# Performance work log

Measured on AMD Instinct MI355X. Metric: run time of the kernel, lower is better.

Reference implementation:

```python
import jax, jax.numpy as jnp
import numpy as np
from jax import lax

NUM_HEADS = 8
NUM_SELECTS = 10
CLIP = 10.0  # tanh logit clipping in pointer-style SingleHeadAttention
NEG = -1e9   # finite -inf substitute (safe under autodiff)


def setup_inputs() -> dict:
    key = jax.random.key(0)
    ks = jax.random.split(key, 8)
    B, N, D = 64, 2048, 256
    s = 1.0 / np.sqrt(D)
    return {
        "encoder_output": jax.random.normal(ks[0], (B, N, D), jnp.float32),
        "in_proj_w": jax.random.uniform(ks[1], (3 * D, D), jnp.float32, -s, s),
        "in_proj_b": jnp.zeros((3 * D,), jnp.float32),
        "out_w": jax.random.uniform(ks[2], (D, D), jnp.float32, -s, s),
        "out_b": jnp.zeros((D,), jnp.float32),
        "sha_wq": jax.random.uniform(ks[3], (D, D), jnp.float32, -s, s),
        "sha_wk": jax.random.uniform(ks[4], (D, D), jnp.float32, -s, s),
        "is_training": False,
    }


def reference(encoder_output, in_proj_w, in_proj_b, out_w, out_b, sha_wq, sha_wk, is_training):
    B, N, D = encoder_output.shape
    H, dh, S = NUM_HEADS, D // NUM_HEADS, NUM_SELECTS
    Wq, Wk, Wv = in_proj_w[:D], in_proj_w[D:2 * D], in_proj_w[2 * D:]
    bq, bk, bv = in_proj_b[:D], in_proj_b[D:2 * D], in_proj_b[2 * D:]

    h_mean = jnp.mean(encoder_output, axis=1)                         # [B,D]
    # MHA query is constant across steps; K/V projections of the encoder too.
    q = (h_mean @ Wq.T + bq).reshape(B, H, dh)                        # [B,H,dh]
    k = (encoder_output @ Wk.T + bk).reshape(B, N, H, dh)             # [B,N,H,dh]
    v = (encoder_output @ Wv.T + bv).reshape(B, N, H, dh)             # [B,N,H,dh]
    ksingle = encoder_output @ sha_wk.T                               # [B,N,D]
    scale = 1.0 / np.sqrt(dh)
    scale2 = 1.0 / np.sqrt(D)
    bidx = jnp.arange(B)

    def step(mask, _):
        # multi-head cross attention, key_padding_mask = mask
        s_mha = jnp.einsum('bhd,bnhd->bhn', q, k) * scale             # [B,H,N]
        s_mha = jnp.where(mask[:, None, :], NEG, s_mha)
        a = jax.nn.softmax(s_mha, axis=-1)
        ctx = jnp.einsum('bhn,bnhd->bhd', a, v).reshape(B, D)
        attn_out = ctx @ out_w.T + out_b                              # [B,D]
        # single-head pointer attention with tanh clipping
        qs = attn_out @ sha_wq.T                                      # [B,D]
        u = CLIP * jnp.tanh(jnp.einsum('bd,bnd->bn', qs, ksingle) * scale2)
        u = jnp.where(mask, NEG, u)                                   # [B,N]
        logp = jax.nn.log_softmax(u, axis=-1)
        p = jnp.exp(logp)
        ent = -jnp.sum(jnp.where(p > 0, p * logp, 0.0), axis=-1)
        # is_training=False path: greedy argmax (deterministic reference)
        idx = jnp.argmax(p, axis=-1)                                  # [B]
        pi_s = p[bidx, idx]
        new_mask = mask.at[bidx, idx].set(True)
        return new_mask, (idx, pi_s, ent)

    mask0 = jnp.zeros((B, N), dtype=bool)
    _, (idxs, pis, ents) = lax.scan(step, mask0, None, length=S)
    selected_clients = idxs.T.astype(jnp.int64 if jax.config.jax_enable_x64 else jnp.int32)  # [B,S]
    pi = pis.T                                                        # [B,S]
    entropy = jnp.sum(ents, axis=0)                                   # [B]
    return selected_clients, pi, entropy
```

## Files before the change

kernel.cpp:

```cpp
#include <hip/hip_runtime.h>
#include <hip/hip_bf16.h>
#include <math.h>

namespace {
constexpr int Bc = 64, Nc = 2048, Dc = 256, Hc = 8, DHc = 32, Sc = 10;
constexpr float kNeg = -1000000000.0f;
constexpr float kClip = 10.0f;
constexpr float kScale = 0.17677669529663687f;
constexpr float kScale2 = 0.0625f;
}

__global__ __launch_bounds__(256) void k_hmean_part(const float* __restrict__ enc,
                                                    float* __restrict__ hpart) {
  int b = blockIdx.x >> 3, c = blockIdx.x & 7, t = threadIdx.x;
  int lane = t & 63, wv = t >> 6;
  __shared__ __align__(16) float part[4][Dc];
  const float4* p = reinterpret_cast<const float4*>(
      enc + ((size_t)b * Nc + c * 256 + wv * 64) * Dc) + lane;
  float4 s; s.x = 0.f; s.y = 0.f; s.z = 0.f; s.w = 0.f;
  #pragma unroll 8
  for (int i = 0; i < 64; ++i) {
    const float4 e = p[(size_t)i * 64];
    s.x += e.x; s.y += e.y; s.z += e.z; s.w += e.w;
  }
  *reinterpret_cast<float4*>(&part[wv][lane * 4]) = s;
  __syncthreads();
  hpart[(size_t)blockIdx.x * Dc + t] =
      part[0][t] + part[1][t] + part[2][t] + part[3][t];
}

__global__ __launch_bounds__(256) void k_qgc(const float* __restrict__ hpart,
                                             const float* __restrict__ w_in,
                                             const float* __restrict__ b_in,
                                             float* __restrict__ g, float* __restrict__ c) {
  int b = blockIdx.x, t = threadIdx.x;
  __shared__ float hm[Dc];
  __shared__ float qsh[Dc];
  {
    float s = 0.f;
    for (int cc = 0; cc < 8; ++cc) s += hpart[(size_t)(b * 8 + cc) * Dc + t];
    hm[t] = s * (1.0f / Nc);
  }
  __syncthreads();
  {
    const float* row = w_in + (size_t)t * Dc;
    float acc = b_in[t];
    for (int d = 0; d < Dc; ++d) acc += row[d] * hm[d];
    qsh[t] = acc;
  }
  __syncthreads();
  for (int h = 0; h < Hc; ++h) {
    float acc = 0.f;
    const float* wk = w_in + (size_t)(Dc + h * DHc) * Dc + t;
    const float* qh = qsh + h * DHc;
    #pragma unroll 8
    for (int i = 0; i < DHc; ++i) acc += qh[i] * wk[(size_t)i * Dc];
    g[((size_t)b * Hc + h) * Dc + t] = acc;
  }
  if (t < Hc) {
    float acc = 0.f;
    for (int i = 0; i < DHc; ++i) acc += qsh[t * DHc + i] * b_in[Dc + t * DHc + i];
    c[b * Hc + t] = acc;
  }
}

__global__ __launch_bounds__(256) void k_A1(const float* __restrict__ swq,
                                            const float* __restrict__ ow,
                                            const float* __restrict__ ob,
                                            float* __restrict__ M1, float* __restrict__ m1b) {
  int i = blockIdx.x, e = threadIdx.x;
  __shared__ float row[Dc];
  __shared__ float red[256];
  row[e] = swq[(size_t)i * Dc + e];
  __syncthreads();
  float acc = 0.f;
  #pragma unroll 4
  for (int k = 0; k < Dc; ++k) acc += row[k] * ow[(size_t)k * Dc + e];
  M1[(size_t)i * Dc + e] = acc;
  red[e] = row[e] * ob[e];
  __syncthreads();
  for (int off = 128; off >= 1; off >>= 1) {
    if (e < off) red[e] += red[e + off];
    __syncthreads();
  }
  if (e == 0) m1b[i] = red[0];
}

__global__ __launch_bounds__(256) void k_A2(const float* __restrict__ swk,
                                            const float* __restrict__ M1,
                                            const float* __restrict__ m1b,
                                            const float* __restrict__ b_in,
                                            float* __restrict__ Aout, float* __restrict__ cvec) {
  int d = blockIdx.x, e = threadIdx.x;
  __shared__ float col[Dc];
  __shared__ float red[256];
  col[e] = swk[(size_t)e * Dc + d];
  __syncthreads();
  float acc = 0.f;
  #pragma unroll 4
  for (int k = 0; k < Dc; ++k) acc += col[k] * M1[(size_t)k * Dc + e];
  Aout[(size_t)d * Dc + e] = acc;
  red[e] = acc * b_in[2 * Dc + e] + col[e] * m1b[e];
  __syncthreads();
  for (int off = 128; off >= 1; off >>= 1) {
    if (e < off) red[e] += red[e + off];
    __syncthreads();
  }
  if (e == 0) cvec[d] = red[0];
}

__global__ __launch_bounds__(256) void k_A3(const float* __restrict__ Aout,
                                            const float* __restrict__ w_in,
                                            float* __restrict__ BT) {
  int h = blockIdx.x >> 3, et = blockIdx.x & 7, d = threadIdx.x;
  float arow[DHc];
  #pragma unroll
  for (int i = 0; i < DHc; ++i) arow[i] = Aout[(size_t)d * Dc + h * DHc + i];
  __shared__ float wv[DHc][DHc];
  for (int k = threadIdx.x; k < DHc * DHc; k += 256) {
    int i = k >> 5, j = k & 31;
    wv[i][j] = w_in[(size_t)(2 * Dc + h * DHc + i) * Dc + et * DHc + j];
  }
  __syncthreads();
  for (int j = 0; j < DHc; ++j) {
    float acc = 0.f;
    #pragma unroll
    for (int i = 0; i < DHc; ++i) acc += arow[i] * wv[i][j];
    BT[((size_t)h * Dc + et * DHc + j) * Dc + d] = acc;
  }
}

__global__ __launch_bounds__(256) void k_scores(const float* __restrict__ enc,
                                                const float* __restrict__ g,
                                                const float* __restrict__ c,
                                                float* __restrict__ s) {
  int b = blockIdx.x >> 4, nt = blockIdx.x & 15, t = threadIdx.x;
  __shared__ __align__(16) float gsm[Hc * Dc];
  __shared__ float csm[Hc];
  for (int k = t; k < Hc * Dc; k += 256) gsm[k] = g[(size_t)b * Hc * Dc + k];
  if (t < Hc) csm[t] = c[b * Hc + t];
  __syncthreads();
  int row = t >> 1, half = t & 1;
  int n = nt * 128 + row;
  const float4* rowp = reinterpret_cast<const float4*>(enc + ((size_t)b * Nc + n) * Dc);
  float acc[Hc] = {};
  #pragma unroll 8
  for (int i = 0; i < 32; ++i) {
    int d4 = i * 2 + half;
    const float4 e = rowp[d4];
    #pragma unroll
    for (int h = 0; h < Hc; ++h) {
      const float4 g4 = *reinterpret_cast<const float4*>(gsm + h * Dc + d4 * 4);
      acc[h] += e.x * g4.x + e.y * g4.y + e.z * g4.z + e.w * g4.w;
    }
  }
  #pragma unroll
  for (int h = 0; h < Hc; ++h) acc[h] += __shfl_xor(acc[h], 1);
  if (half == 0) {
    #pragma unroll
    for (int h = 0; h < Hc; ++h)
      s[((size_t)b * Hc + h) * Nc + n] = kScale * (acc[h] + csm[h]);
  }
}

__global__ __launch_bounds__(256) void k_rowmax(const float* __restrict__ s,
                                                float* __restrict__ mrow) {
  int bh = blockIdx.x, t = threadIdx.x;
  __shared__ float red[256];
  float m = -3.0e38f;
  #pragma unroll
  for (int q = 0; q < 8; ++q) m = fmaxf(m, s[(size_t)bh * Nc + q * 256 + t]);
  red[t] = m;
  __syncthreads();
  for (int off = 128; off >= 1; off >>= 1) {
    if (t < off) red[t] = fmaxf(red[t], red[t + off]);
    __syncthreads();
  }
  if (t == 0) mrow[bh] = red[0];
}

__global__ __launch_bounds__(256) void k_S0part(const float* __restrict__ enc,
                                                const float* __restrict__ s,
                                                const float* __restrict__ mrow,
                                                float* __restrict__ w,
                                                float* __restrict__ Spart) {
  int b = blockIdx.x >> 3, cid = blockIdx.x & 7, t = threadIdx.x;
  __shared__ __align__(16) float wsmT[256 * 8];
  __shared__ __align__(16) float part[4][Hc][Dc];
  {
    float eh[8];
    #pragma unroll
    for (int h = 0; h < Hc; ++h) {
      float m = mrow[b * Hc + h];
      float e = expf(s[((size_t)b * Hc + h) * Nc + cid * 256 + t] - m);
      eh[h] = e;
      w[((size_t)b * Hc + h) * Nc + cid * 256 + t] = e;
    }
    float4 v0; v0.x = eh[0]; v0.y = eh[1]; v0.z = eh[2]; v0.w = eh[3];
    float4 v1; v1.x = eh[4]; v1.y = eh[5]; v1.z = eh[6]; v1.w = eh[7];
    *reinterpret_cast<float4*>(&wsmT[t * 8]) = v0;
    *reinterpret_cast<float4*>(&wsmT[t * 8 + 4]) = v1;
  }
  __syncthreads();
  int lane = t & 63, wv = t >> 6;
  float4 acc[Hc];
  #pragma unroll
  for (int h = 0; h < Hc; ++h) { acc[h].x = 0.f; acc[h].y = 0.f; acc[h].z = 0.f; acc[h].w = 0.f; }
  const float4* ep = reinterpret_cast<const float4*>(
      enc + ((size_t)b * Nc + cid * 256 + wv * 64) * Dc) + lane;
  for (int i = 0; i < 64; ++i) {
    const float4 e4 = ep[(size_t)i * 64];
    int row = wv * 64 + i;
    const float4 w0 = *reinterpret_cast<const float4*>(&wsmT[row * 8]);
    const float4 w1 = *reinterpret_cast<const float4*>(&wsmT[row * 8 + 4]);
    const float wh[8] = {w0.x, w0.y, w0.z, w0.w, w1.x, w1.y, w1.z, w1.w};
    #pragma unroll
    for (int h = 0; h < Hc; ++h) {
      acc[h].x += wh[h] * e4.x; acc[h].y += wh[h] * e4.y;
      acc[h].z += wh[h] * e4.z; acc[h].w += wh[h] * e4.w;
    }
  }
  #pragma unroll
  for (int h = 0; h < Hc; ++h)
    *reinterpret_cast<float4*>(&part[wv][h][lane * 4]) = acc[h];
  __syncthreads();
  #pragma unroll
  for (int h = 0; h < Hc; ++h)
    Spart[(((size_t)b * 8 + cid) * Hc + h) * Dc + t] =
        part[0][h][t] + part[1][h][t] + part[2][h][t] + part[3][h][t];
}

__global__ __launch_bounds__(256) void k_S0red(const float* __restrict__ Spart,
                                               const float* __restrict__ w,
                                               float* __restrict__ Sacc,
                                               float* __restrict__ W0) {
  int b = blockIdx.x >> 3, h = blockIdx.x & 7, t = threadIdx.x;
  __shared__ float red[256];
  float acc = 0.f;
  for (int cid = 0; cid < 8; ++cid)
    acc += Spart[(((size_t)b * 8 + cid) * Hc + h) * Dc + t];
  Sacc[((size_t)b * Hc + h) * Dc + t] = acc;
  float ws = 0.f;
  #pragma unroll
  for (int q = 0; q < 8; ++q) ws += w[((size_t)b * Hc + h) * Nc + q * 256 + t];
  red[t] = ws;
  __syncthreads();
  for (int off = 128; off >= 1; off >>= 1) {
    if (t < off) red[t] += red[t + off];
    __syncthreads();
  }
  if (t == 0) W0[b * Hc + h] = red[0];
}

__device__ __forceinline__ void select_core(const float* __restrict__ ub,
                                            const int* histsh, int nhist, int t,
                                            float* red, int* redi,
                                            int& gidx_out, float& lse_out, float& ent_out) {
  float uval[8];
  float lmax = -3.0e38f;
  int lidx = 0;
  #pragma unroll
  for (int q = 0; q < 8; ++q) {
    int n = t + q * 256;
    float v = ub[n];
    for (int tt = 0; tt < nhist; ++tt)
      if (n == histsh[tt]) v = kNeg;
    uval[q] = v;
    if (v > lmax) { lmax = v; lidx = n; }
  }
  red[t] = lmax; redi[t] = lidx;
  __syncthreads();
  for (int off = 128; off >= 1; off >>= 1) {
    if (t < off) {
      float o = red[t + off]; int oi = redi[t + off];
      if (o > red[t] || (o == red[t] && oi < redi[t])) { red[t] = o; redi[t] = oi; }
    }
    __syncthreads();
  }
  float mu = red[0];
  int gidx = redi[0];
  __syncthreads();
  float ssum = 0.f;
  #pragma unroll
  for (int q = 0; q < 8; ++q) ssum += expf(uval[q] - mu);
  red[t] = ssum;
  __syncthreads();
  for (int off = 128; off >= 1; off >>= 1) {
    if (t < off) red[t] += red[t + off];
    __syncthreads();
  }
  float Z = red[0];
  float lse = mu + logf(Z);
  __syncthreads();
  float ent = 0.f;
  #pragma unroll
  for (int q = 0; q < 8; ++q) {
    float logp = uval[q] - lse;
    float p = expf(logp);
    if (p > 0.f) ent -= p * logp;
  }
  red[t] = ent;
  __syncthreads();
  for (int off = 128; off >= 1; off >>= 1) {
    if (t < off) red[t] += red[t + off];
    __syncthreads();
  }
  ent_out = red[0];
  gidx_out = gidx;
  lse_out = lse;
  __syncthreads();
}

__global__ __launch_bounds__(256) void k_selchain(const float* __restrict__ u,
                                                  int* __restrict__ hist,
                                                  float* __restrict__ out,
                                                  const float* __restrict__ Sacc,
                                                  const float* __restrict__ W0,
                                                  const float* __restrict__ w,
                                                  const float* __restrict__ enc,
                                                  const float* __restrict__ BT,
                                                  float* __restrict__ rpart, int tstep) {
  int b = blockIdx.x >> 3, h = blockIdx.x & 7, t = threadIdx.x;
  __shared__ float red[256];
  __shared__ int redi[256];
  __shared__ int histsh[16];
  __shared__ float sh[Dc];
  if (t < 16) histsh[t] = (t < tstep - 1) ? hist[b * 16 + t] : -1;
  __syncthreads();

  if (tstep > 0) {
    int sel_t = tstep - 1;
    int gidx; float lse, ent;
    select_core(u + (size_t)b * Nc, histsh, sel_t, t, red, redi, gidx, lse, ent);
    if (h == 0 && t == 0) {
      float pi = expf(u[(size_t)b * Nc + gidx] - lse);
      out[b * Sc + sel_t] = (float)gidx;
      out[Bc * Sc + b * Sc + sel_t] = pi;
      if (sel_t == 0) out[2 * Bc * Sc + b] = ent;
      else out[2 * Bc * Sc + b] += ent;
      hist[b * 16 + sel_t] = gidx;
    }
    if (t == 0) histsh[sel_t] = gidx;
    __syncthreads();
  }

  float se = Sacc[((size_t)b * Hc + h) * Dc + t];
  float Wh = W0[b * Hc + h];
  for (int tt = 0; tt < tstep; ++tt) {
    int j = histsh[tt];
    float wv = w[((size_t)b * Hc + h) * Nc + j];
    se -= wv * enc[((size_t)b * Nc + j) * Dc + t];
    Wh -= wv;
  }
  sh[t] = se / Wh;
  __syncthreads();
  const float* bt = BT + (size_t)h * Dc * Dc + t;
  float a0 = 0.f, a1 = 0.f, a2 = 0.f, a3 = 0.f;
  #pragma unroll 4
  for (int e = 0; e < Dc; e += 4) {
    a0 += bt[(size_t)e * Dc] * sh[e];
    a1 += bt[(size_t)(e + 1) * Dc] * sh[e + 1];
    a2 += bt[(size_t)(e + 2) * Dc] * sh[e + 2];
    a3 += bt[(size_t)(e + 3) * Dc] * sh[e + 3];
  }
  rpart[((size_t)b * Hc + h) * Dc + t] = (a0 + a1) + (a2 + a3);
}

__global__ __launch_bounds__(256) void k_uscore(const float* __restrict__ enc,
                                                const float* __restrict__ rpart,
                                                const float* __restrict__ cvec,
                                                float* __restrict__ u) {
  int b = blockIdx.x >> 5, ng = blockIdx.x & 31, t = threadIdx.x;
  __shared__ __align__(16) float rsm[Dc];
  {
    float vsum = cvec[t];
    #pragma unroll
    for (int h = 0; h < Hc; ++h) vsum += rpart[((size_t)b * Hc + h) * Dc + t];
    rsm[t] = vsum;
  }
  __syncthreads();
  int row = t >> 2, q = t & 3;
  int n = ng * 64 + row;
  const float4* rowp = reinterpret_cast<const float4*>(enc + ((size_t)b * Nc + n) * Dc);
  const float4* r4 = reinterpret_cast<const float4*>(rsm);
  float acc = 0.f;
  #pragma unroll
  for (int i = 0; i < 16; ++i) {
    int d4 = i * 4 + q;
    const float4 e = rowp[d4];
    const float4 rr = r4[d4];
    acc += e.x * rr.x + e.y * rr.y + e.z * rr.z + e.w * rr.w;
  }
  acc += __shfl_xor(acc, 1);
  acc += __shfl_xor(acc, 2);
  if (q == 0) u[(size_t)b * Nc + n] = kClip * tanhf(kScale2 * acc);
}

__global__ __launch_bounds__(256) void k_selfinal(const float* __restrict__ u,
                                                  const int* __restrict__ hist,
                                                  float* __restrict__ out) {
  int b = blockIdx.x, t = threadIdx.x;
  __shared__ float red[256];
  __shared__ int redi[256];
  __shared__ int histsh[16];
  if (t < 16) histsh[t] = (t < Sc - 1) ? hist[b * 16 + t] : -1;
  __syncthreads();
  int gidx; float lse, ent;
  select_core(u + (size_t)b * Nc, histsh, Sc - 1, t, red, redi, gidx, lse, ent);
  if (t == 0) {
    float pi = expf(u[(size_t)b * Nc + gidx] - lse);
    out[b * Sc + (Sc - 1)] = (float)gidx;
    out[Bc * Sc + b * Sc + (Sc - 1)] = pi;
    out[2 * Bc * Sc + b] += ent;
  }
}

extern "C" void kernel_launch(void* const* d_in, const int* in_sizes, int n_in,
                              void* d_out, int out_size, void* d_ws, size_t ws_size,
                              hipStream_t stream) {
  (void)in_sizes; (void)n_in; (void)out_size; (void)ws_size;
  const float* enc  = (const float*)d_in[0];
  const float* in_w = (const float*)d_in[1];
  const float* in_b = (const float*)d_in[2];
  const float* ow   = (const float*)d_in[3];
  const float* ob   = (const float*)d_in[4];
  const float* swq  = (const float*)d_in[5];
  const float* swk  = (const float*)d_in[6];
  float* out = (float*)d_out;

  float* ws = (float*)d_ws;
  size_t off = 0;
  auto alloc = [&](size_t n) { float* p = ws + off; off += n; return p; };
  float* hpart = alloc((size_t)Bc * 8 * Dc);
  float* g     = alloc((size_t)Bc * Hc * Dc);
  float* c     = alloc((size_t)Bc * Hc);
  float* s     = alloc((size_t)Bc * Hc * Nc);
  float* mrow  = alloc((size_t)Bc * Hc);
  float* w     = alloc((size_t)Bc * Hc * Nc);
  float* W0    = alloc((size_t)Bc * Hc);
  float* Spart = alloc((size_t)Bc * 8 * Hc * Dc);
  float* Sacc  = alloc((size_t)Bc * Hc * Dc);
  float* M1    = alloc((size_t)Dc * Dc);
  float* m1b   = alloc(Dc);
  float* Aout  = alloc((size_t)Dc * Dc);
  float* cvec  = alloc(Dc);
  float* BT    = alloc((size_t)Hc * Dc * Dc);
  float* rpart = alloc((size_t)Bc * Hc * Dc);
  float* u     = alloc((size_t)Bc * Nc);
  int* hist    = (int*)alloc((size_t)Bc * 16);

  k_hmean_part<<<Bc * 8, 256, 0, stream>>>(enc, hpart);
  k_qgc<<<Bc, 256, 0, stream>>>(hpart, in_w, in_b, g, c);
  k_A1<<<Dc, 256, 0, stream>>>(swq, ow, ob, M1, m1b);
  k_A2<<<Dc, 256, 0, stream>>>(swk, M1, m1b, in_b, Aout, cvec);
  k_A3<<<Hc * 8, 256, 0, stream>>>(Aout, in_w, BT);
  k_scores<<<Bc * 16, 256, 0, stream>>>(enc, g, c, s);
  k_rowmax<<<Bc * Hc, 256, 0, stream>>>(s, mrow);
  k_S0part<<<Bc * 8, 256, 0, stream>>>(enc, s, mrow, w, Spart);
  k_S0red<<<Bc * Hc, 256, 0, stream>>>(Spart, w, Sacc, W0);

  for (int t = 0; t < Sc; ++t) {
    k_selchain<<<Bc * Hc, 256, 0, stream>>>(u, hist, out, Sacc, W0, w, enc, BT, rpart, t);
    k_uscore<<<Bc * 32, 256, 0, stream>>>(enc, rpart, cvec, u);
  }
  k_selfinal<<<Bc, 256, 0, stream>>>(u, hist, out);
}
```

Measured before the change: 508.7 us.

## Fuse score, rowmax and weighted-sum kernels using per-chunk online softmax rescaling

Merges the MHA score computation, global row max, and exp-weighted encoder accumulation into one kernel that uses a chunk-local max per block, then rescales partial sums and weights in the reduction kernel (flash-style). This removes the intermediate score buffer round trip and two kernel launches, and lets the encoder chunk be reread while still hot in cache. In exchange, each thread now reads a full 1KB row alone in the score phase, which gives less coalesced loads, and the reduction kernel does an extra read-modify-write of w.

```diff
diff --git a/kernel.cpp b/kernel.cpp
--- a/kernel.cpp
+++ b/kernel.cpp
@@ -130,71 +130,64 @@
   }
 }
 
-__global__ __launch_bounds__(256) void k_scores(const float* __restrict__ enc,
-                                                const float* __restrict__ g,
-                                                const float* __restrict__ c,
-                                                float* __restrict__ s) {
-  int b = blockIdx.x >> 4, nt = blockIdx.x & 15, t = threadIdx.x;
+__global__ __launch_bounds__(256) void k_scoreS0(const float* __restrict__ enc,
+                                                 const float* __restrict__ g,
+                                                 const float* __restrict__ c,
+                                                 float* __restrict__ w,
+                                                 float* __restrict__ Spart,
+                                                 float* __restrict__ mrowc) {
+  int b = blockIdx.x >> 3, cid = blockIdx.x & 7, t = threadIdx.x;
+  int lane = t & 63, wvi = t >> 6;
   __shared__ __align__(16) float gsm[Hc * Dc];
   __shared__ float csm[Hc];
+  __shared__ __align__(16) float wsmT[256 * 8];
+  __shared__ __align__(16) float part[4][Hc][Dc];
+  __shared__ float wmax[4][Hc];
   for (int k = t; k < Hc * Dc; k += 256) gsm[k] = g[(size_t)b * Hc * Dc + k];
   if (t < Hc) csm[t] = c[b * Hc + t];
   __syncthreads();
-  int row = t >> 1, half = t & 1;
-  int n = nt * 128 + row;
-  const float4* rowp = reinterpret_cast<const float4*>(enc + ((size_t)b * Nc + n) * Dc);
-  float acc[Hc] = {};
-  #pragma unroll 8
-  for (int i = 0; i < 32; ++i) {
-    int d4 = i * 2 + half;
-    const float4 e = rowp[d4];
+
+  int n = cid * 256 + t;
+  float sv[Hc];
+  {
+    const float4* rowp = reinterpret_cast<const float4*>(enc + ((size_t)b * Nc + n) * Dc);
+    float acc[Hc] = {};
+    #pragma unroll 8
+    for (int d4 = 0; d4 < 64; ++d4) {
+      const float4 e = rowp[d4];
+      #pragma unroll
+      for (int h = 0; h < Hc; ++h) {
+        const float4 g4 = *reinterpret_cast<const float4*>(gsm + h * Dc + d4 * 4);
+        acc[h] += e.x * g4.x + e.y * g4.y + e.z * g4.z + e.w * g4.w;
+      }
+    }
+    #pragma unroll
+    for (int h = 0; h < Hc; ++h) sv[h] = kScale * (acc[h] + csm[h]);
+  }
+  {
+    float wm[Hc];
     #pragma unroll
     for (int h = 0; h < Hc; ++h) {
-      const float4 g4 = *reinterpret_cast<const float4*>(gsm + h * Dc + d4 * 4);
-      acc[h] += e.x * g4.x + e.y * g4.y + e.z * g4.z + e.w * g4.w;
-    }
-  }
-  #pragma unroll
-  for (int h = 0; h < Hc; ++h) acc[h] += __shfl_xor(acc[h], 1);
-  if (half == 0) {
-    #pragma unroll
-    for (int h = 0; h < Hc; ++h)
-      s[((size_t)b * Hc + h) * Nc + n] = kScale * (acc[h] + csm[h]);
-  }
-}
-
-__global__ __launch_bounds__(256) void k_rowmax(const float* __restrict__ s,
-                                                float* __restrict__ mrow) {
-  int bh = blockIdx.x, t = threadIdx.x;
-  __shared__ float red[256];
-  float m = -3.0e38f;
-  #pragma unroll
-  for (int q = 0; q < 8; ++q) m = fmaxf(m, s[(size_t)bh * Nc + q * 256 + t]);
-  red[t] = m;
-  __syncthreads();
-  for (int off = 128; off >= 1; off >>= 1) {
-    if (t < off) red[t] = fmaxf(red[t], red[t + off]);
-    __syncthreads();
-  }
-  if (t == 0) mrow[bh] = red[0];
-}
-
-__global__ __launch_bounds__(256) void k_S0part(const float* __restrict__ enc,
-                                                const float* __restrict__ s,
-                                                const float* __restrict__ mrow,
-                                                float* __restrict__ w,
-                                                float* __restrict__ Spart) {
-  int b = blockIdx.x >> 3, cid = blockIdx.x & 7, t = threadIdx.x;
-  __shared__ __align__(16) float wsmT[256 * 8];
-  __shared__ __align__(16) float part[4][Hc][Dc];
-  {
-    float eh[8];
+      float m = sv[h];
+      #pragma unroll
+      for (int off = 32; off >= 1; off >>= 1) m = fmaxf(m, __shfl_xor(m, off));
+      wm[h] = m;
+    }
+    if (lane == 0) {
+      #pragma unroll
+      for (int h = 0; h < Hc; ++h) wmax[wvi][h] = wm[h];
+    }
+  }
+  __syncthreads();
+  {
+    float eh[Hc];
     #pragma unroll
     for (int h = 0; h < Hc; ++h) {
-      float m = mrow[b * Hc + h];
-      float e = expf(s[((size_t)b * Hc + h) * Nc + cid * 256 + t] - m);
+      float mc = fmaxf(fmaxf(wmax[0][h], wmax[1][h]), fmaxf(wmax[2][h], wmax[3][h]));
+      float e = expf(sv[h] - mc);
       eh[h] = e;
-      w[((size_t)b * Hc + h) * Nc + cid * 256 + t] = e;
+      w[((size_t)b * Hc + h) * Nc + n] = e;
+      if (t == 0) mrowc[((size_t)b * 8 + cid) * Hc + h] = mc;
     }
     float4 v0; v0.x = eh[0]; v0.y = eh[1]; v0.z = eh[2]; v0.w = eh[3];
     float4 v1; v1.x = eh[4]; v1.y = eh[5]; v1.z = eh[6]; v1.w = eh[7];
@@ -202,27 +195,27 @@
     *reinterpret_cast<float4*>(&wsmT[t * 8 + 4]) = v1;
   }
   __syncthreads();
-  int lane = t & 63, wv = t >> 6;
-  float4 acc[Hc];
-  #pragma unroll
-  for (int h = 0; h < Hc; ++h) { acc[h].x = 0.f; acc[h].y = 0.f; acc[h].z = 0.f; acc[h].w = 0.f; }
+
+  float4 acc2[Hc];
+  #pragma unroll
+  for (int h = 0; h < Hc; ++h) { acc2[h].x = 0.f; acc2[h].y = 0.f; acc2[h].z = 0.f; acc2[h].w = 0.f; }
   const float4* ep = reinterpret_cast<const float4*>(
-      enc + ((size_t)b * Nc + cid * 256 + wv * 64) * Dc) + lane;
+      enc + ((size_t)b * Nc + cid * 256 + wvi * 64) * Dc) + lane;
   for (int i = 0; i < 64; ++i) {
     const float4 e4 = ep[(size_t)i * 64];
-    int row = wv * 64 + i;
+    int row = wvi * 64 + i;
     const float4 w0 = *reinterpret_cast<const float4*>(&wsmT[row * 8]);
     const float4 w1 = *reinterpret_cast<const float4*>(&wsmT[row * 8 + 4]);
     const float wh[8] = {w0.x, w0.y, w0.z, w0.w, w1.x, w1.y, w1.z, w1.w};
     #pragma unroll
     for (int h = 0; h < Hc; ++h) {
-      acc[h].x += wh[h] * e4.x; acc[h].y += wh[h] * e4.y;
-      acc[h].z += wh[h] * e4.z; acc[h].w += wh[h] * e4.w;
+      acc2[h].x += wh[h] * e4.x; acc2[h].y += wh[h] * e4.y;
+      acc2[h].z += wh[h] * e4.z; acc2[h].w += wh[h] * e4.w;
     }
   }
   #pragma unroll
   for (int h = 0; h < Hc; ++h)
-    *reinterpret_cast<float4*>(&part[wv][h][lane * 4]) = acc[h];
+    *reinterpret_cast<float4*>(&part[wvi][h][lane * 4]) = acc2[h];
   __syncthreads();
   #pragma unroll
   for (int h = 0; h < Hc; ++h)
@@ -231,18 +224,34 @@
 }
 
 __global__ __launch_bounds__(256) void k_S0red(const float* __restrict__ Spart,
-                                               const float* __restrict__ w,
+                                               const float* __restrict__ mrowc,
+                                               float* __restrict__ w,
                                                float* __restrict__ Sacc,
                                                float* __restrict__ W0) {
   int b = blockIdx.x >> 3, h = blockIdx.x & 7, t = threadIdx.x;
   __shared__ float red[256];
+  float mc[8], m = -3.0e38f;
+  #pragma unroll
+  for (int cd = 0; cd < 8; ++cd) {
+    mc[cd] = mrowc[((size_t)b * 8 + cd) * Hc + h];
+    m = fmaxf(m, mc[cd]);
+  }
+  float f[8];
+  #pragma unroll
+  for (int cd = 0; cd < 8; ++cd) f[cd] = expf(mc[cd] - m);
   float acc = 0.f;
-  for (int cid = 0; cid < 8; ++cid)
-    acc += Spart[(((size_t)b * 8 + cid) * Hc + h) * Dc + t];
+  #pragma unroll
+  for (int cd = 0; cd < 8; ++cd)
+    acc += Spart[(((size_t)b * 8 + cd) * Hc + h) * Dc + t] * f[cd];
   Sacc[((size_t)b * Hc + h) * Dc + t] = acc;
   float ws = 0.f;
   #pragma unroll
-  for (int q = 0; q < 8; ++q) ws += w[((size_t)b * Hc + h) * Nc + q * 256 + t];
+  for (int q = 0; q < 8; ++q) {
+    size_t idx = ((size_t)b * Hc + h) * Nc + q * 256 + t;
+    float v = w[idx] * f[q];
+    w[idx] = v;
+    ws += v;
+  }
   red[t] = ws;
   __syncthreads();
   for (int off = 128; off >= 1; off >>= 1) {
@@ -434,11 +443,10 @@
   float* hpart = alloc((size_t)Bc * 8 * Dc);
   float* g     = alloc((size_t)Bc * Hc * Dc);
   float* c     = alloc((size_t)Bc * Hc);
-  float* s     = alloc((size_t)Bc * Hc * Nc);
-  float* mrow  = alloc((size_t)Bc * Hc);
   float* w     = alloc((size_t)Bc * Hc * Nc);
   float* W0    = alloc((size_t)Bc * Hc);
   float* Spart = alloc((size_t)Bc * 8 * Hc * Dc);
+  float* mrowc = alloc((size_t)Bc * 8 * Hc);
   float* Sacc  = alloc((size_t)Bc * Hc * Dc);
   float* M1    = alloc((size_t)Dc * Dc);
   float* m1b   = alloc(Dc);
@@ -454,10 +462,8 @@
   k_A1<<<Dc, 256, 0, stream>>>(swq, ow, ob, M1, m1b);
   k_A2<<<Dc, 256, 0, stream>>>(swk, M1, m1b, in_b, Aout, cvec);
   k_A3<<<Hc * 8, 256, 0, stream>>>(Aout, in_w, BT);
-  k_scores<<<Bc * 16, 256, 0, stream>>>(enc, g, c, s);
-  k_rowmax<<<Bc * Hc, 256, 0, stream>>>(s, mrow);
-  k_S0part<<<Bc * 8, 256, 0, stream>>>(enc, s, mrow, w, Spart);
-  k_S0red<<<Bc * Hc, 256, 0, stream>>>(Spart, w, Sacc, W0);
+  k_scoreS0<<<Bc * 8, 256, 0, stream>>>(enc, g, c, w, Spart, mrowc);
+  k_S0red<<<Bc * Hc, 256, 0, stream>>>(Spart, mrowc, w, Sacc, W0);
 
   for (int t = 0; t < Sc; ++t) {
     k_selchain<<<Bc * Hc, 256, 0, stream>>>(u, hist, out, Sacc, W0, w, enc, BT, rpart, t);
```

Result: no change. 506.9 us (-0.4%).
